# Optimization experiments

Hardware: AMD Instinct MI355X
Metric: run time of the kernel (lower is better)

The kernel has to match this reference:

```python
import jax, jax.numpy as jnp
import numpy as np

B, S, H, NH, DH, DFF = 4, 8192, 2048, 16, 128, 8192
K = 1024
EPS = 1e-5
THETA = 10000.0
SCALE_FACTOR = 1.0
SCALE_GAP = 1.0


def setup_inputs() -> dict:
    key = jax.random.key(0)
    ks = jax.random.split(key, 12)
    hidden_states = jax.random.normal(ks[0], (B, S, H), dtype=jnp.float32)
    position_ids = jnp.broadcast_to(jnp.arange(S, dtype=jnp.int32)[None, :], (B, S))
    # exactly K routed tokens per row -> static compacted length (matches torch
    # path when all rows have equal top-k counts)
    rowkeys = jax.random.split(ks[1], B)
    sel = jax.vmap(lambda k: jax.random.permutation(k, S)[:K])(rowkeys)  # [B,K]
    topk_mask = jnp.zeros((B, S), dtype=bool).at[jnp.arange(B)[:, None], sel].set(True)
    topk_scores = jax.random.uniform(ks[2], (B,), dtype=jnp.float32)
    w = lambda k, shp: (jax.random.normal(k, shp, dtype=jnp.float32) * 0.02)
    return {
        "hidden_states": hidden_states,
        "position_ids": position_ids,
        "topk_mask": topk_mask,
        "topk_scores": topk_scores,
        "topk_k": K,
        "Wq": w(ks[3], (H, H)),
        "Wk": w(ks[4], (H, H)),
        "Wv": w(ks[5], (H, H)),
        "Wo": w(ks[6], (H, H)),
        "Wgate": w(ks[7], (H, DFF)),
        "Wup": w(ks[8], (H, DFF)),
        "Wdown": w(ks[9], (DFF, H)),
        "ln1_w": jnp.ones((H,), dtype=jnp.float32),
        "ln2_w": jnp.ones((H,), dtype=jnp.float32),
    }


def _rmsnorm(x, w):
    return x * jax.lax.rsqrt(jnp.mean(x * x, axis=-1, keepdims=True) + EPS) * w


def _rotate_half(x):
    x1, x2 = jnp.split(x, 2, axis=-1)
    return jnp.concatenate([-x2, x1], axis=-1)


def reference(hidden_states, position_ids, topk_mask, topk_scores, topk_k,
              Wq, Wk, Wv, Wo, Wgate, Wup, Wdown, ln1_w, ln2_w):
    Kk = int(topk_k)
    b, s, h = hidden_states.shape
    # true positions first, in original order (stable) -> compacted indices
    order = jnp.argsort(jnp.where(topk_mask, 0, 1).astype(jnp.int32), axis=1, stable=True)
    topk_idx = order[:, :Kk]                              # [B,K]
    bidx = jnp.arange(b)[:, None]
    # 🔍 dispatch: gather routed tokens into compact [B,K,H]
    x = hidden_states[bidx, topk_idx]
    pos = position_ids[bidx, topk_idx]                    # original positions for RoPE

    residual = x
    hs = _rmsnorm(x, ln1_w)
    q = (hs @ Wq).reshape(b, Kk, NH, DH).transpose(0, 2, 1, 3)
    k = (hs @ Wk).reshape(b, Kk, NH, DH).transpose(0, 2, 1, 3)
    v = (hs @ Wv).reshape(b, Kk, NH, DH).transpose(0, 2, 1, 3)
    inv_freq = 1.0 / (THETA ** (jnp.arange(0, DH, 2, dtype=jnp.float32) / DH))
    freqs = pos[..., None].astype(jnp.float32) * inv_freq  # [B,K,DH/2]
    emb = jnp.concatenate([freqs, freqs], axis=-1)
    cos = jnp.cos(emb)[:, None, :, :]
    sin = jnp.sin(emb)[:, None, :, :]
    q = q * cos + _rotate_half(q) * sin
    k = k * cos + _rotate_half(k) * sin
    scores = jnp.einsum('bhqd,bhkd->bhqk', q, k) / np.sqrt(DH).astype(np.float32)
    causal = jnp.tril(jnp.ones((Kk, Kk), dtype=bool))
    scores = jnp.where(causal, scores, jnp.finfo(scores.dtype).min)
    attn = jax.nn.softmax(scores, axis=-1)
    o = jnp.einsum('bhqk,bhkd->bhqd', attn, v).transpose(0, 2, 1, 3).reshape(b, Kk, H)
    hs = residual + o @ Wo

    residual2 = hs
    m = _rmsnorm(hs, ln2_w)
    m = (jax.nn.silu(m @ Wgate) * (m @ Wup)) @ Wdown

    # rescale_hidden_states=True path
    scale = 0.5 * SCALE_FACTOR + (topk_scores - 0.5) * SCALE_GAP  # [B]
    out_gathered = residual2 + m * scale[:, None, None]
    # 🔍 combine: scatter routed outputs back; bottom tokens pass through unchanged
    out = hidden_states.at[bidx, topk_idx].set(out_gathered)
    return out
```

## Files before the change

### kernel.cpp

```cpp
#include <hip/hip_runtime.h>
#include <hip/hip_bf16.h>
#include <stdint.h>

#define Bb 4
#define Ss 8192
#define Hh 2048
#define NHh 16
#define DHh 128
#define DFFf 8192
#define KS 1024
#define NTOK 4096

typedef unsigned short u16;
typedef __bf16 bf16x8 __attribute__((ext_vector_type(8)));
typedef float f32x4 __attribute__((ext_vector_type(4)));

union B8 { uint4 u; bf16x8 v; u16 s[8]; };

__device__ __forceinline__ float b2f(u16 x) { return __uint_as_float(((unsigned)x) << 16); }
__device__ __forceinline__ u16 f2b(float x) {
  __hip_bfloat16 h = __float2bfloat16(x);
  return *reinterpret_cast<u16*>(&h);
}

__device__ __forceinline__ void gll16(const void* g, void* l) {
  __builtin_amdgcn_global_load_lds((const __attribute__((address_space(1))) void*)g,
                                   (__attribute__((address_space(3))) void*)l, 16, 0, 0);
}

__device__ __forceinline__ int swz16(int r, int cg) {
  int u = ((r & 1) << 2) | cg;
  return ((r >> 1) << 3) | (u ^ ((r >> 1) & 7));
}

__global__ void topk_prep(const void* maskp, const int* __restrict__ posids,
                          const float* __restrict__ scores,
                          int* __restrict__ idx, int* __restrict__ posg,
                          float* __restrict__ scalev) {
  int b = blockIdx.x;
  int tid = threadIdx.x, lane = tid & 63, wv = tid >> 6;
  __shared__ int wsum[4];
  __shared__ int base;
  __shared__ int mode;
  __shared__ int detCnt;
  if (tid == 0) { base = 0; detCnt = 0; }
  __syncthreads();
  {
    const unsigned char* mb = (const unsigned char*)maskp;
    int c = 0;
    for (int s = tid; s < 8192; s += 256) c += (mb[s] != 0);
    atomicAdd(&detCnt, c);
  }
  __syncthreads();
  if (tid == 0) mode = (detCnt == KS) ? 1 : 0;
  __syncthreads();
  const unsigned char* mb = (const unsigned char*)maskp;
  const int* mi = (const int*)maskp;
  for (int s0 = 0; s0 < Ss; s0 += 256) {
    int s = s0 + tid;
    int pred = mode ? (mb[(size_t)b * Ss + s] != 0) : (mi[(size_t)b * Ss + s] != 0);
    unsigned long long bal = __ballot(pred);
    int lp = __popcll(bal & ((1ull << lane) - 1ull));
    int wtot = __popcll(bal);
    if (lane == 0) wsum[wv] = wtot;
    __syncthreads();
    int woff = 0;
    for (int w = 0; w < wv; ++w) woff += wsum[w];
    int tot = wsum[0] + wsum[1] + wsum[2] + wsum[3];
    int p = base + woff + lp;
    if (pred && p < KS) {
      idx[b * KS + p] = s;
      posg[b * KS + p] = posids[(size_t)b * Ss + s];
    }
    __syncthreads();
    if (tid == 0) base += tot;
    __syncthreads();
  }
  if (b == 0 && tid < Bb) scalev[tid] = 0.5f * 1.0f + (scores[tid] - 0.5f) * 1.0f;
}

template <int MODE>
__global__ void transpose_w(const float* __restrict__ in, u16* __restrict__ out, int R, int C) {
  __shared__ float tile[32][33];
  int tx = threadIdx.x, ty = threadIdx.y;
  int c0 = blockIdx.x * 32, r0 = blockIdx.y * 32;
  for (int j = ty; j < 32; j += 8) tile[j][tx] = in[(size_t)(r0 + j) * C + c0 + tx];
  __syncthreads();
  for (int j = ty; j < 32; j += 8) {
    int c = c0 + j;
    size_t row = (MODE == 0) ? c : (size_t)((c >> 5) << 6) + (c & 31) + (MODE == 2 ? 32 : 0);
    out[row * R + r0 + tx] = f2b(tile[tx][j]);
  }
}

template <int GATHER>
__global__ __launch_bounds__(256) void rmsnorm_k(const float* __restrict__ src0,
                                                 const int* __restrict__ idx,
                                                 const float* __restrict__ w,
                                                 u16* __restrict__ out) {
  int t = blockIdx.x;
  const float* src;
  if (GATHER) { int b = t >> 10; src = src0 + ((size_t)b * Ss + idx[t]) * Hh; }
  else src = src0 + (size_t)t * Hh;
  int tid = threadIdx.x, lane = tid & 63, wv = tid >> 6;
  float4 x0 = *(const float4*)(src + tid * 8);
  float4 x1 = *(const float4*)(src + tid * 8 + 4);
  float ss = x0.x * x0.x + x0.y * x0.y + x0.z * x0.z + x0.w * x0.w +
             x1.x * x1.x + x1.y * x1.y + x1.z * x1.z + x1.w * x1.w;
  for (int o = 32; o; o >>= 1) ss += __shfl_down(ss, o);
  __shared__ float wred[4];
  if (lane == 0) wred[wv] = ss;
  __syncthreads();
  float tot = wred[0] + wred[1] + wred[2] + wred[3];
  float r = rsqrtf(tot * (1.0f / Hh) + 1e-5f);
  const float* wp = w + tid * 8;
  u16* op = out + (size_t)t * Hh + tid * 8;
  float xs[8] = {x0.x, x0.y, x0.z, x0.w, x1.x, x1.y, x1.z, x1.w};
#pragma unroll
  for (int j = 0; j < 8; ++j) op[j] = f2b(xs[j] * r * wp[j]);
}

template <int EPI>
__global__ __launch_bounds__(512, 2) void gemm256(
    const u16* __restrict__ A, const u16* __restrict__ Bt,
    int N, int Kd, int lda, int gm, int gw, int nb,
    u16* __restrict__ Cb,
    const float* __restrict__ hid, const int* __restrict__ idx,
    const float* __restrict__ hs2, const float* __restrict__ scalev,
    float* __restrict__ Cf) {
  __shared__ u16 lds[65536];
  int bid = blockIdx.x;
  int xcd = bid & 7;
  int i2 = bid >> 3;
  int bm = i2 / gw;
  int bn = xcd * gw + i2 % gw + nb;
  int m0 = bm * 256, n0 = bn * 256;
  int tid = threadIdx.x, lane = tid & 63, wv = tid >> 6;
  int wm = wv >> 2, wn = wv & 3;
  int NT = Kd >> 6;

  int P16 = wv * 64 + lane;
  int blk = P16 >> 3, up = P16 & 7;
  int uu = up ^ (blk & 7);
  int r0 = blk * 2 + (uu >> 2), cg0 = uu & 3;
  const u16* srcA = A + (size_t)(m0 + r0) * lda + cg0 * 8;
  const u16* srcB = Bt + (size_t)(n0 + r0) * Kd + cg0 * 8;
  size_t rsA = (size_t)128 * lda, rsB = (size_t)128 * Kd;

  int offA = swz16(wm * 128 + (lane & 15), lane >> 4) * 8;
  int offB = 32768 + swz16(wn * 64 + (lane & 15), lane >> 4) * 8;
  u16* ldsw = &lds[wv * 512];

  f32x4 acc[8][4] = {};
  B8 aR[4], bR[4];

  gll16(srcB,      ldsw + 32768); gll16(srcB + rsB,      ldsw + 36864);
  gll16(srcA,      ldsw +     0); gll16(srcA + rsA,      ldsw +  4096);
  gll16(srcB + 32, ldsw + 40960); gll16(srcB + 32 + rsB, ldsw + 45056);
  gll16(srcA + 32, ldsw +  8192); gll16(srcA + 32 + rsA, ldsw + 12288);
  gll16(srcB + 64, ldsw + 49152); gll16(srcB + 64 + rsB, ldsw + 53248);
  gll16(srcA + 64, ldsw + 16384); gll16(srcA + 64 + rsA, ldsw + 20480);
  gll16(srcB + 96, ldsw + 57344); gll16(srcB + 96 + rsB, ldsw + 61440);
  asm volatile("s_waitcnt vmcnt(6)" ::: "memory");
  asm volatile("s_barrier" ::: "memory");

  const u16* stA = srcA + 64;
  const u16* stB = srcB + 64;

  auto phase = [&](int abase, int bbase, int mh) {
    if (mh == 0) {
#pragma unroll
      for (int nf = 0; nf < 4; ++nf) bR[nf].u = *(const uint4*)&lds[offB + bbase + nf * 512];
    }
#pragma unroll
    for (int i3 = 0; i3 < 4; ++i3)
      aR[i3].u = *(const uint4*)&lds[offA + abase + (i3 + 4 * mh) * 512];
  };
  auto mfma16 = [&](int mh) {
    asm volatile("s_barrier" ::: "memory");
    asm volatile("s_waitcnt lgkmcnt(0)" ::: "memory");
    __builtin_amdgcn_s_setprio(1);
#pragma unroll
    for (int nf = 0; nf < 4; ++nf)
#pragma unroll
      for (int i3 = 0; i3 < 4; ++i3)
        acc[mh * 4 + i3][nf] =
            __builtin_amdgcn_mfma_f32_16x16x32_bf16(aR[i3].v, bR[nf].v, acc[mh * 4 + i3][nf], 0, 0, 0);
    __builtin_amdgcn_s_setprio(0);
  };

  for (int ktp = 0; ktp < NT; ktp += 2) {
    bool sAll = (ktp < NT - 2);
    phase(0, 0, 0);
    { gll16(stA + 32, ldsw + 24576); gll16(stA + 32 + rsA, ldsw + 28672); }
    mfma16(0);
    asm volatile("s_barrier" ::: "memory");
    phase(0, 0, 1);
    if (sAll) { gll16(stB + 64, ldsw + 32768); gll16(stB + 64 + rsB, ldsw + 36864); }
    mfma16(1);
    asm volatile("s_barrier" ::: "memory");
    phase(8192, 8192, 0);
    if (sAll) { gll16(stA + 64, ldsw + 0); gll16(stA + 64 + rsA, ldsw + 4096); }
    mfma16(0);
    asm volatile("s_barrier" ::: "memory");
    phase(8192, 8192, 1);
    if (sAll) { gll16(stB + 96, ldsw + 40960); gll16(stB + 96 + rsB, ldsw + 45056); }
    mfma16(1);
    if (sAll) asm volatile("s_waitcnt vmcnt(6)" ::: "memory");
    else asm volatile("s_waitcnt vmcnt(0)" ::: "memory");
    asm volatile("s_barrier" ::: "memory");
    phase(16384, 16384, 0);
    if (sAll) { gll16(stA + 96, ldsw + 8192); gll16(stA + 96 + rsA, ldsw + 12288); }
    mfma16(0);
    asm volatile("s_barrier" ::: "memory");
    phase(16384, 16384, 1);
    if (sAll) { gll16(stB + 128, ldsw + 49152); gll16(stB + 128 + rsB, ldsw + 53248); }
    mfma16(1);
    asm volatile("s_barrier" ::: "memory");
    phase(24576, 24576, 0);
    if (sAll) { gll16(stA + 128, ldsw + 16384); gll16(stA + 128 + rsA, ldsw + 20480); }
    mfma16(0);
    asm volatile("s_barrier" ::: "memory");
    phase(24576, 24576, 1);
    if (sAll) { gll16(stB + 160, ldsw + 57344); gll16(stB + 160 + rsB, ldsw + 61440); }
    mfma16(1);
    if (sAll) asm volatile("s_waitcnt vmcnt(6)" ::: "memory");
    asm volatile("s_barrier" ::: "memory");
    stA += 128; stB += 128;
  }

  if (EPI == 4) {
    int gcol0 = ((n0 + wn * 64) >> 1) + (lane & 15);
#pragma unroll
    for (int mf = 0; mf < 8; ++mf) {
#pragma unroll
      for (int rr = 0; rr < 4; ++rr) {
        int row = m0 + wm * 128 + mf * 16 + (lane >> 4) * 4 + rr;
#pragma unroll
        for (int nf = 0; nf < 2; ++nf) {
          float g = acc[mf][nf][rr];
          float u = acc[mf][nf + 2][rr];
          Cb[(size_t)row * 8192 + gcol0 + nf * 16] = f2b(g / (1.0f + __expf(-g)) * u);
        }
      }
    }
    return;
  }

#pragma unroll
  for (int mf = 0; mf < 8; ++mf) {
#pragma unroll
    for (int rr = 0; rr < 4; ++rr) {
      int row = m0 + wm * 128 + mf * 16 + (lane >> 4) * 4 + rr;
#pragma unroll
      for (int nf = 0; nf < 4; ++nf) {
        int col = n0 + wn * 64 + nf * 16 + (lane & 15);
        float v = acc[mf][nf][rr];
        if (EPI == 0) {
          Cb[(size_t)row * N + col] = f2b(v);
        } else if (EPI == 1) {
          int b = row >> 10;
          Cf[(size_t)row * Hh + col] = hid[((size_t)b * Ss + idx[row]) * Hh + col] + v;
        } else {
          int b = row >> 10;
          Cf[((size_t)b * Ss + idx[row]) * Hh + col] = hs2[(size_t)row * Hh + col] + v * scalev[b];
        }
      }
    }
  }
}

template <int EPI>
__global__ __launch_bounds__(512, 4) void gemm128(
    const u16* __restrict__ A, const u16* __restrict__ Bt,
    int N, int Kd, int lda, int gm, int gw,
    u16* __restrict__ Cb,
    const float* __restrict__ hid, const int* __restrict__ idx,
    const float* __restrict__ hs2, const float* __restrict__ scalev,
    float* __restrict__ Cf, u16* __restrict__ vTout) {
  __shared__ u16 lds[36864];
  int bid = blockIdx.x;
  int xcd = bid & 7;
  int i2 = bid >> 3;
  int bm = i2 / gw;
  int bn = xcd * gw + i2 % gw;
  int m0 = bm * 128, n0 = bn * 256;
  int tid = threadIdx.x, lane = tid & 63, wv = tid >> 6;
  int wm = wv >> 2, wn = wv & 3;
  int NT = Kd >> 6;
  int P = NT * 2;

  int P16 = wv * 64 + lane;
  int blk = P16 >> 3, up = P16 & 7;
  int uu = up ^ (blk & 7);
  int r0 = blk * 2 + (uu >> 2), cg0 = uu & 3;
  const u16* srcA = A + (size_t)(m0 + r0) * lda + cg0 * 8;
  const u16* srcB = Bt + (size_t)(n0 + r0) * Kd + cg0 * 8;
  size_t rsB = (size_t)128 * Kd;

  int offB = swz16(wn * 64 + (lane & 15), lane >> 4) * 8;
  int offA = swz16(wm * 64 + (lane & 15), lane >> 4) * 8;
  u16* ldsw = &lds[wv * 512];

  f32x4 acc[4][4] = {};
  B8 aR[4], bR[4];

  auto stage = [&](int q, int bB, int aB) {
    const u16* spB = srcB + q * 32;
    gll16(spB, ldsw + bB);
    gll16(spB + rsB, ldsw + bB + 4096);
    gll16(srcA + q * 32, ldsw + aB);
  };

  stage(0, 0, 24576);
  stage(1, 8192, 28672);
  asm volatile("s_waitcnt vmcnt(3)" ::: "memory");
  asm volatile("s_barrier" ::: "memory");

  int rB = 0, rA = 24576;
  int tB = 16384, tA = 32768;
  for (int p = 0; p < P; ++p) {
#pragma unroll
    for (int f = 0; f < 4; ++f) bR[f].u = *(const uint4*)&lds[rB + offB + f * 512];
#pragma unroll
    for (int f = 0; f < 4; ++f) aR[f].u = *(const uint4*)&lds[rA + offA + f * 512];
    if (p + 2 < P) stage(p + 2, tB, tA);
    asm volatile("s_barrier" ::: "memory");
    asm volatile("s_waitcnt lgkmcnt(0)" ::: "memory");
    __builtin_amdgcn_s_setprio(1);
#pragma unroll
    for (int nf = 0; nf < 4; ++nf)
#pragma unroll
      for (int mf = 0; mf < 4; ++mf)
        acc[mf][nf] = __builtin_amdgcn_mfma_f32_16x16x32_bf16(aR[mf].v, bR[nf].v, acc[mf][nf], 0, 0, 0);
    __builtin_amdgcn_s_setprio(0);
    if (p < P - 2) asm volatile("s_waitcnt vmcnt(3)" ::: "memory");
    else if (p == P - 2) asm volatile("s_waitcnt vmcnt(0)" ::: "memory");
    asm volatile("s_barrier" ::: "memory");
    tB = rB; tA = rA;
    rB = (rB == 16384) ? 0 : rB + 8192;
    rA = (rA == 32768) ? 24576 : rA + 4096;
  }

  if (EPI == 3) {
#pragma unroll
    for (int mf = 0; mf < 4; ++mf) {
      int rowb = m0 + wm * 64 + mf * 16 + (lane >> 4) * 4;
      int bb = rowb >> 10, kk2 = rowb & 1023;
      int w = kk2 & 127;
      int kk2p = (kk2 & ~127) | (((((w >> 5) & 3) << 2) + ((w >> 2) & 3)) << 3) | (((w >> 4) & 1) << 2);
#pragma unroll
      for (int nf = 0; nf < 4; ++nf) {
        int col = n0 + wn * 64 + nf * 16 + (lane & 15);
        if (col >= 4096) {
          int hh = (col - 4096) >> 7, dd = (col - 4096) & 127;
          ushort4 pk;
          pk.x = f2b(acc[mf][nf][0]); pk.y = f2b(acc[mf][nf][1]);
          pk.z = f2b(acc[mf][nf][2]); pk.w = f2b(acc[mf][nf][3]);
          *(ushort4*)&vTout[(((size_t)bb * 16 + hh) * 128 + dd) * 1024 + kk2p] = pk;
        } else {
#pragma unroll
          for (int rr = 0; rr < 4; ++rr)
            Cb[(size_t)(rowb + rr) * N + col] = f2b(acc[mf][nf][rr]);
        }
      }
    }
    return;
  }

#pragma unroll
  for (int mf = 0; mf < 4; ++mf) {
#pragma unroll
    for (int rr = 0; rr < 4; ++rr) {
      int row = m0 + wm * 64 + mf * 16 + (lane >> 4) * 4 + rr;
#pragma unroll
      for (int nf = 0; nf < 4; ++nf) {
        int col = n0 + wn * 64 + nf * 16 + (lane & 15);
        float v = acc[mf][nf][rr];
        if (EPI == 0) {
          Cb[(size_t)row * N + col] = f2b(v);
        } else if (EPI == 1) {
          int b = row >> 10;
          Cf[(size_t)row * Hh + col] = hid[((size_t)b * Ss + idx[row]) * Hh + col] + v;
        } else {
          int b = row >> 10;
          Cf[((size_t)b * Ss + idx[row]) * Hh + col] = hs2[(size_t)row * Hh + col] + v * scalev[b];
        }
      }
    }
  }
}

__global__ __launch_bounds__(256) void rope_qk(u16* __restrict__ qkv,
                                               const int* __restrict__ posg) {
  int gid = blockIdx.x * 256 + threadIdx.x;
  int i = gid & 63;
  int h = (gid >> 6) & 15;
  int t = gid >> 10;
  float p = (float)posg[t];
  float inv = exp2f(-(float)i * (13.287712379549449f / 64.0f));
  float ang = p * inv;
  float sv, cv;
  __sincosf(ang, &sv, &cv);
  size_t base = (size_t)t * 6144 + h * DHh + i;
  u16* Q = qkv;
  u16* Kq = qkv + 2048;
  float q1 = b2f(Q[base]), q2 = b2f(Q[base + 64]);
  Q[base] = f2b(q1 * cv - q2 * sv);
  Q[base + 64] = f2b(q2 * cv + q1 * sv);
  float k1 = b2f(Kq[base]), k2 = b2f(Kq[base + 64]);
  Kq[base] = f2b(k1 * cv - k2 * sv);
  Kq[base + 64] = f2b(k2 * cv + k1 * sv);
}

__global__ __launch_bounds__(256) void attn_k(const u16* __restrict__ QKV,
                                              const u16* __restrict__ vT,
                                              u16* __restrict__ O) {
  int qb = blockIdx.x;
  int head = blockIdx.y;
  int b = head >> 4, h = head & 15;
  int tid = threadIdx.x, lane = tid & 63, wv = tid >> 6;
  int l15 = lane & 15, lq = lane >> 4, l7 = lane & 7;
  __shared__ __align__(16) u16 KsA[16384];
  __shared__ __align__(16) u16 VtA[16384];

  int rr0 = tid >> 4;
  int u0 = tid & 15;
  size_t koff0 = (size_t)rr0 * 6144 + ((u0 ^ (rr0 & 7)) * 8);
  size_t voff0 = (size_t)rr0 * 1024 + ((u0 ^ (rr0 & 7)) * 8);
  char* dK = (char*)KsA + wv * 1024;
  char* dV = (char*)VtA + wv * 1024;

  int q0 = qb * 64 + wv * 16;
  int tokQ = b * KS + q0;
  B8 qf[4];
  const u16* qp = QKV + (size_t)(tokQ + l15) * 6144 + h * DHh;
#pragma unroll
  for (int c = 0; c < 4; ++c) qf[c].u = *(const uint4*)(qp + c * 32 + lq * 8);
  float m_run = -1e30f, l_run = 0.0f;
  f32x4 oacc[8] = {};
  int qi = q0 + l15;

  int nt = (qb >> 1) + 1;
  for (int t = 0; t < nt; ++t) {
    int ks = t * 128;
    bool maskTile = (t == nt - 1);
    __syncthreads();
    const u16* kp = QKV + (size_t)(b * KS + ks) * 6144 + 2048 + h * DHh + koff0;
    const u16* vp = vT + (size_t)head * 131072 + ks + voff0;
#pragma unroll
    for (int i = 0; i < 8; ++i) gll16(kp + (size_t)i * 98304, dK + i * 4096);
#pragma unroll
    for (int i = 0; i < 8; ++i) gll16(vp + i * 16384, dV + i * 4096);
    asm volatile("s_waitcnt vmcnt(8)" ::: "memory");
    __syncthreads();
    f32x4 st[8] = {};
#pragma unroll
    for (int c = 0; c < 4; ++c) {
#pragma unroll
      for (int kt = 0; kt < 8; ++kt) {
        B8 kf;
        kf.u = *(const uint4*)&KsA[(kt * 16 + l15) * 128 + (((c * 4 + lq) ^ l7) * 8)];
        st[kt] = __builtin_amdgcn_mfma_f32_16x16x32_bf16(kf.v, qf[c].v, st[kt], 0, 0, 0);
      }
    }
    float pmax = -INFINITY;
    if (maskTile) {
#pragma unroll
      for (int kt = 0; kt < 8; ++kt)
#pragma unroll
        for (int r = 0; r < 4; ++r) {
          int ki = ks + kt * 16 + lq * 4 + r;
          float v = st[kt][r] * 0.088388347648318447f;
          v = (ki <= qi) ? v : -INFINITY;
          st[kt][r] = v;
          pmax = fmaxf(pmax, v);
        }
    } else {
#pragma unroll
      for (int kt = 0; kt < 8; ++kt)
#pragma unroll
        for (int r = 0; r < 4; ++r) {
          float v = st[kt][r] * 0.088388347648318447f;
          st[kt][r] = v;
          pmax = fmaxf(pmax, v);
        }
    }
    pmax = fmaxf(pmax, __shfl_xor(pmax, 16));
    pmax = fmaxf(pmax, __shfl_xor(pmax, 32));
    float m_new = fmaxf(m_run, pmax);
    float alpha = __expf(m_run - m_new);
    float psum = 0.0f;
#pragma unroll
    for (int kt = 0; kt < 8; ++kt)
#pragma unroll
      for (int r = 0; r < 4; ++r) {
        float pv = __expf(st[kt][r] - m_new);
        st[kt][r] = pv;
        psum += pv;
      }
    psum += __shfl_xor(psum, 16);
    psum += __shfl_xor(psum, 32);
    l_run = l_run * alpha + psum;
    m_run = m_new;
    asm volatile("s_waitcnt vmcnt(0)" ::: "memory");
    __syncthreads();
    B8 pf[4];
#pragma unroll
    for (int kslot = 0; kslot < 4; ++kslot)
#pragma unroll
      for (int j = 0; j < 4; ++j) {
        pf[kslot].s[j] = f2b(st[2 * kslot][j]);
        pf[kslot].s[4 + j] = f2b(st[2 * kslot + 1][j]);
      }
    float al0 = __shfl(alpha, lq * 4 + 0);
    float al1 = __shfl(alpha, lq * 4 + 1);
    float al2 = __shfl(alpha, lq * 4 + 2);
    float al3 = __shfl(alpha, lq * 4 + 3);
#pragma unroll
    for (int dt = 0; dt < 8; ++dt) {
      oacc[dt][0] *= al0; oacc[dt][1] *= al1;
      oacc[dt][2] *= al2; oacc[dt][3] *= al3;
    }
#pragma unroll
    for (int dt = 0; dt < 8; ++dt) {
      int d = dt * 16 + l15;
#pragma unroll
      for (int kslot = 0; kslot < 4; ++kslot) {
        B8 vf;
        vf.u = *(const uint4*)&VtA[d * 128 + (((kslot * 4 + lq) ^ l7) * 8)];
        oacc[dt] = __builtin_amdgcn_mfma_f32_16x16x32_bf16(pf[kslot].v, vf.v, oacc[dt], 0, 0, 0);
      }
    }
  }
  float linv = 1.0f / l_run;
  float li[4];
#pragma unroll
  for (int r = 0; r < 4; ++r) li[r] = __shfl(linv, lq * 4 + r);
#pragma unroll
  for (int r = 0; r < 4; ++r) {
    int tok = tokQ + lq * 4 + r;
    u16* op = O + (size_t)tok * Hh + h * DHh;
#pragma unroll
    for (int dt = 0; dt < 8; ++dt) op[dt * 16 + l15] = f2b(oacc[dt][r] * li[r]);
  }
}

extern "C" void kernel_launch(void* const* d_in, const int* in_sizes, int n_in,
                              void* d_out, int out_size, void* d_ws, size_t ws_size,
                              hipStream_t stream) {
  (void)in_sizes; (void)n_in; (void)out_size; (void)ws_size;
  const float* hid = (const float*)d_in[0];
  const int* posids = (const int*)d_in[1];
  const void* mask = d_in[2];
  const float* scores = (const float*)d_in[3];
  const float* Wq = (const float*)d_in[5];
  const float* Wk = (const float*)d_in[6];
  const float* Wv = (const float*)d_in[7];
  const float* Wo = (const float*)d_in[8];
  const float* Wg = (const float*)d_in[9];
  const float* Wu = (const float*)d_in[10];
  const float* Wd = (const float*)d_in[11];
  const float* ln1 = (const float*)d_in[12];
  const float* ln2 = (const float*)d_in[13];
  float* out = (float*)d_out;
  char* ws = (char*)d_ws;

  u16* WqkvT = (u16*)(ws + 0);
  u16* WoT   = (u16*)(ws + 25165824);
  u16* WguT  = (u16*)(ws + 33554432);
  u16* WdT   = (u16*)(ws + 100663296);
  int* idx   = (int*)(ws + 134217728);
  int* posg  = (int*)(ws + 134217728 + 16384);
  float* scalev = (float*)(ws + 134217728 + 32768);
  char* R = ws + 134283264;
  u16* hsn    = (u16*)(R);
  u16* qkv    = (u16*)(R + 16777216);
  u16* attn_o = (u16*)(R + 67108864);
  u16* vT     = (u16*)(R + 88080384);
  u16* gu2    = (u16*)(R);
  float* hs2  = (float*)(ws + 268500992);
  u16* mnorm  = (u16*)(ws + 302055424);

  hipMemcpyAsync(out, hid, (size_t)Bb * Ss * Hh * 4, hipMemcpyDeviceToDevice, stream);

  topk_prep<<<Bb, 256, 0, stream>>>(mask, posids, scores, idx, posg, scalev);

  transpose_w<0><<<dim3(64, 64), dim3(32, 8), 0, stream>>>(Wq, WqkvT, 2048, 2048);
  transpose_w<0><<<dim3(64, 64), dim3(32, 8), 0, stream>>>(Wk, WqkvT + 2048 * 2048, 2048, 2048);
  transpose_w<0><<<dim3(64, 64), dim3(32, 8), 0, stream>>>(Wv, WqkvT + 4096 * 2048, 2048, 2048);
  transpose_w<0><<<dim3(64, 64), dim3(32, 8), 0, stream>>>(Wo, WoT, 2048, 2048);
  transpose_w<1><<<dim3(256, 64), dim3(32, 8), 0, stream>>>(Wg, WguT, 2048, 8192);
  transpose_w<2><<<dim3(256, 64), dim3(32, 8), 0, stream>>>(Wu, WguT, 2048, 8192);
  transpose_w<0><<<dim3(64, 256), dim3(32, 8), 0, stream>>>(Wd, WdT, 8192, 2048);

  rmsnorm_k<1><<<NTOK, 256, 0, stream>>>(hid, idx, ln1, hsn);

  gemm128<3><<<768, 512, 0, stream>>>(hsn, WqkvT, 6144, 2048, 2048, 32, 3, qkv,
                                      nullptr, nullptr, nullptr, nullptr, nullptr, vT);

  rope_qk<<<16384, 256, 0, stream>>>(qkv, posg);

  attn_k<<<dim3(16, 64), 256, 0, stream>>>(qkv, vT, attn_o);

  gemm128<1><<<256, 512, 0, stream>>>(attn_o, WoT, 2048, 2048, 2048, 32, 1, nullptr,
                                      hid, idx, nullptr, nullptr, hs2, nullptr);

  rmsnorm_k<0><<<NTOK, 256, 0, stream>>>(hs2, nullptr, ln2, mnorm);

  gemm256<4><<<512, 512, 0, stream>>>(mnorm, WguT, 16384, 2048, 2048, 16, 4, 0, gu2,
                                      nullptr, nullptr, nullptr, nullptr, nullptr);
  gemm256<4><<<512, 512, 0, stream>>>(mnorm, WguT, 16384, 2048, 2048, 16, 4, 32, gu2,
                                      nullptr, nullptr, nullptr, nullptr, nullptr);

  gemm128<2><<<256, 512, 0, stream>>>(gu2, WdT, 2048, 8192, 8192, 32, 1, nullptr,
                                      nullptr, idx, hs2, scalev, out, nullptr);
}
```

Baseline: 1.035 ms.

## Vectorize weight transpose and RoPE, remap GEMM tiles, merge gate/up GEMM launches

Rewrites the weight transpose so each block handles 64 rows and each thread writes eight packed bf16 values as one 16-byte store, and vectorizes RoPE so each thread rotates four adjacent elements with ushort4 loads and stores. Adds an optional 2D tile mapping across XCDs in gemm128, used for the output and down projections, to improve L2 reuse. Merges the two gate/up GEMM launches into one 1024-block launch. These target narrow memory accesses, launch overhead and cache locality, at the cost of more registers per thread in RoPE and transpose.

```diff
diff --git a/kernel.cpp b/kernel.cpp
--- a/kernel.cpp
+++ b/kernel.cpp
@@ -80,17 +80,24 @@
 }
 
 template <int MODE>
-__global__ void transpose_w(const float* __restrict__ in, u16* __restrict__ out, int R, int C) {
-  __shared__ float tile[32][33];
-  int tx = threadIdx.x, ty = threadIdx.y;
-  int c0 = blockIdx.x * 32, r0 = blockIdx.y * 32;
-  for (int j = ty; j < 32; j += 8) tile[j][tx] = in[(size_t)(r0 + j) * C + c0 + tx];
+__global__ __launch_bounds__(256) void transpose_w(const float* __restrict__ in,
+                                                   u16* __restrict__ out, int R, int C) {
+  __shared__ float tile[64][33];
+  int t = threadIdx.x;
+  int c0 = blockIdx.x * 32, r0 = blockIdx.y * 64;
+  int tx = t & 31, ty = t >> 5;
+#pragma unroll
+  for (int j = 0; j < 8; ++j)
+    tile[j * 8 + ty][tx] = in[(size_t)(r0 + j * 8 + ty) * C + c0 + tx];
   __syncthreads();
-  for (int j = ty; j < 32; j += 8) {
-    int c = c0 + j;
-    size_t row = (MODE == 0) ? c : (size_t)((c >> 5) << 6) + (c & 31) + (MODE == 2 ? 32 : 0);
-    out[row * R + r0 + tx] = f2b(tile[tx][j]);
-  }
+  int c = t >> 3, g = t & 7;
+  int cc = c0 + c;
+  size_t row = (MODE == 0) ? (size_t)cc
+                           : (size_t)((cc >> 5) << 6) + (cc & 31) + (MODE == 2 ? 32 : 0);
+  B8 pk;
+#pragma unroll
+  for (int k = 0; k < 8; ++k) pk.s[k] = f2b(tile[g * 8 + k][c]);
+  *(uint4*)&out[row * R + r0 + g * 8] = pk.u;
 }
 
 template <int GATHER>
@@ -273,7 +280,7 @@
 template <int EPI>
 __global__ __launch_bounds__(512, 4) void gemm128(
     const u16* __restrict__ A, const u16* __restrict__ Bt,
-    int N, int Kd, int lda, int gm, int gw,
+    int N, int Kd, int lda, int gm, int gw, int r2d,
     u16* __restrict__ Cb,
     const float* __restrict__ hid, const int* __restrict__ idx,
     const float* __restrict__ hs2, const float* __restrict__ scalev,
@@ -282,8 +289,15 @@
   int bid = blockIdx.x;
   int xcd = bid & 7;
   int i2 = bid >> 3;
-  int bm = i2 / gw;
-  int bn = xcd * gw + i2 % gw;
+  int bm, bn;
+  if (r2d) {
+    int xr = xcd >> 1, xc = xcd & 1;
+    bm = xr * 8 + (i2 & 7);
+    bn = xc * 4 + (i2 >> 3);
+  } else {
+    bm = i2 / gw;
+    bn = xcd * gw + i2 % gw;
+  }
   int m0 = bm * 128, n0 = bn * 256;
   int tid = threadIdx.x, lane = tid & 63, wv = tid >> 6;
   int wm = wv >> 2, wn = wv & 3;
@@ -394,23 +408,32 @@
 __global__ __launch_bounds__(256) void rope_qk(u16* __restrict__ qkv,
                                                const int* __restrict__ posg) {
   int gid = blockIdx.x * 256 + threadIdx.x;
-  int i = gid & 63;
-  int h = (gid >> 6) & 15;
-  int t = gid >> 10;
+  int i4 = (gid & 15) << 2;
+  int h = (gid >> 4) & 15;
+  int t = gid >> 8;
   float p = (float)posg[t];
-  float inv = exp2f(-(float)i * (13.287712379549449f / 64.0f));
-  float ang = p * inv;
-  float sv, cv;
-  __sincosf(ang, &sv, &cv);
-  size_t base = (size_t)t * 6144 + h * DHh + i;
+  size_t base = (size_t)t * 6144 + h * DHh + i4;
   u16* Q = qkv;
   u16* Kq = qkv + 2048;
-  float q1 = b2f(Q[base]), q2 = b2f(Q[base + 64]);
-  Q[base] = f2b(q1 * cv - q2 * sv);
-  Q[base + 64] = f2b(q2 * cv + q1 * sv);
-  float k1 = b2f(Kq[base]), k2 = b2f(Kq[base + 64]);
-  Kq[base] = f2b(k1 * cv - k2 * sv);
-  Kq[base + 64] = f2b(k2 * cv + k1 * sv);
+  ushort4 q1 = *(ushort4*)&Q[base], q2 = *(ushort4*)&Q[base + 64];
+  ushort4 k1 = *(ushort4*)&Kq[base], k2 = *(ushort4*)&Kq[base + 64];
+  u16* q1p = (u16*)&q1; u16* q2p = (u16*)&q2;
+  u16* k1p = (u16*)&k1; u16* k2p = (u16*)&k2;
+#pragma unroll
+  for (int j = 0; j < 4; ++j) {
+    int i = i4 + j;
+    float inv = exp2f(-(float)i * (13.287712379549449f / 64.0f));
+    float sv, cv;
+    __sincosf(p * inv, &sv, &cv);
+    float a1 = b2f(q1p[j]), a2 = b2f(q2p[j]);
+    q1p[j] = f2b(a1 * cv - a2 * sv);
+    q2p[j] = f2b(a2 * cv + a1 * sv);
+    float c1 = b2f(k1p[j]), c2 = b2f(k2p[j]);
+    k1p[j] = f2b(c1 * cv - c2 * sv);
+    k2p[j] = f2b(c2 * cv + c1 * sv);
+  }
+  *(ushort4*)&Q[base] = q1; *(ushort4*)&Q[base + 64] = q2;
+  *(ushort4*)&Kq[base] = k1; *(ushort4*)&Kq[base + 64] = k2;
 }
 
 __global__ __launch_bounds__(256) void attn_k(const u16* __restrict__ QKV,
@@ -586,33 +609,31 @@
 
   topk_prep<<<Bb, 256, 0, stream>>>(mask, posids, scores, idx, posg, scalev);
 
-  transpose_w<0><<<dim3(64, 64), dim3(32, 8), 0, stream>>>(Wq, WqkvT, 2048, 2048);
-  transpose_w<0><<<dim3(64, 64), dim3(32, 8), 0, stream>>>(Wk, WqkvT + 2048 * 2048, 2048, 2048);
-  transpose_w<0><<<dim3(64, 64), dim3(32, 8), 0, stream>>>(Wv, WqkvT + 4096 * 2048, 2048, 2048);
-  transpose_w<0><<<dim3(64, 64), dim3(32, 8), 0, stream>>>(Wo, WoT, 2048, 2048);
-  transpose_w<1><<<dim3(256, 64), dim3(32, 8), 0, stream>>>(Wg, WguT, 2048, 8192);
-  transpose_w<2><<<dim3(256, 64), dim3(32, 8), 0, stream>>>(Wu, WguT, 2048, 8192);
-  transpose_w<0><<<dim3(64, 256), dim3(32, 8), 0, stream>>>(Wd, WdT, 8192, 2048);
+  transpose_w<0><<<dim3(64, 32), 256, 0, stream>>>(Wq, WqkvT, 2048, 2048);
+  transpose_w<0><<<dim3(64, 32), 256, 0, stream>>>(Wk, WqkvT + 2048 * 2048, 2048, 2048);
+  transpose_w<0><<<dim3(64, 32), 256, 0, stream>>>(Wv, WqkvT + 4096 * 2048, 2048, 2048);
+  transpose_w<0><<<dim3(64, 32), 256, 0, stream>>>(Wo, WoT, 2048, 2048);
+  transpose_w<1><<<dim3(256, 32), 256, 0, stream>>>(Wg, WguT, 2048, 8192);
+  transpose_w<2><<<dim3(256, 32), 256, 0, stream>>>(Wu, WguT, 2048, 8192);
+  transpose_w<0><<<dim3(64, 128), 256, 0, stream>>>(Wd, WdT, 8192, 2048);
 
   rmsnorm_k<1><<<NTOK, 256, 0, stream>>>(hid, idx, ln1, hsn);
 
-  gemm128<3><<<768, 512, 0, stream>>>(hsn, WqkvT, 6144, 2048, 2048, 32, 3, qkv,
+  gemm128<3><<<768, 512, 0, stream>>>(hsn, WqkvT, 6144, 2048, 2048, 32, 3, 0, qkv,
                                       nullptr, nullptr, nullptr, nullptr, nullptr, vT);
 
-  rope_qk<<<16384, 256, 0, stream>>>(qkv, posg);
+  rope_qk<<<4096, 256, 0, stream>>>(qkv, posg);
 
   attn_k<<<dim3(16, 64), 256, 0, stream>>>(qkv, vT, attn_o);
 
-  gemm128<1><<<256, 512, 0, stream>>>(attn_o, WoT, 2048, 2048, 2048, 32, 1, nullptr,
+  gemm128<1><<<256, 512, 0, stream>>>(attn_o, WoT, 2048, 2048, 2048, 32, 1, 1, nullptr,
                                       hid, idx, nullptr, nullptr, hs2, nullptr);
 
   rmsnorm_k<0><<<NTOK, 256, 0, stream>>>(hs2, nullptr, ln2, mnorm);
 
-  gemm256<4><<<512, 512, 0, stream>>>(mnorm, WguT, 16384, 2048, 2048, 16, 4, 0, gu2,
-                                      nullptr, nullptr, nullptr, nullptr, nullptr);
-  gemm256<4><<<512, 512, 0, stream>>>(mnorm, WguT, 16384, 2048, 2048, 16, 4, 32, gu2,
-                                      nullptr, nullptr, nullptr, nullptr, nullptr);
-
-  gemm128<2><<<256, 512, 0, stream>>>(gu2, WdT, 2048, 8192, 8192, 32, 1, nullptr,
+  gemm256<4><<<1024, 512, 0, stream>>>(mnorm, WguT, 16384, 2048, 2048, 16, 8, 0, gu2,
+                                       nullptr, nullptr, nullptr, nullptr, nullptr);
+
+  gemm128<2><<<256, 512, 0, stream>>>(gu2, WdT, 2048, 8192, 8192, 32, 1, 1, nullptr,
                                       nullptr, idx, hs2, scalev, out, nullptr);
 }
```

Result: faster. 971.7 us (-6.1%).
